# Optimization experiments

Measured on AMD Instinct MI355X. Metric: run time of the kernel, lower is better.

The kernel has to match this reference:

```python
import jax, jax.numpy as jnp
import numpy as np
from jax import lax

# pywt db4 filters. REC_LO is pywt's rec_lo; the others follow pywt's QMF relations:
# rec_hi[k] = (-1)**k * rec_lo[F-1-k]; dec_lo = rec_lo[::-1]; dec_hi = rec_hi[::-1].
REC_LO = np.array([0.23037781330885523, 0.7148465705525415, 0.6308807679295904,
                   -0.027983769416983849, -0.18703481171888114, 0.030841381835986965,
                   0.032883011666982945, -0.010597401784997278], dtype=np.float32)
F = 8
REC_HI = np.array([(-1.0) ** k * REC_LO[F - 1 - k] for k in range(F)], dtype=np.float32)
DEC_LO = REC_LO[::-1].copy()
DEC_HI = REC_HI[::-1].copy()
LEVELS = 3


def _conv(x, kern, stride=1, lhs_dilation=1, padding=((0, 0),)):
    # x: (N, 1, L) ; 1-D correlation (jax conv does NOT flip the kernel)
    k = jnp.asarray(kern, x.dtype).reshape(1, 1, -1)
    return lax.conv_general_dilated(x, k, window_strides=(stride,), padding=padding,
                                    lhs_dilation=(lhs_dilation,),
                                    dimension_numbers=('NCH', 'OIH', 'NCH'))


def dwt(x):
    # pywt single-level dwt, mode='symmetric': extend by F-1 each side, then
    # decimated convolution with dec filters. Equivalent to: drop first extended
    # sample and stride-2 correlate with reversed dec filter (= rec filter).
    xe = jnp.pad(x, ((0, 0), (0, 0), (F - 1, F - 1)), mode='symmetric')[..., 1:]
    cA = _conv(xe, REC_LO, stride=2)   # rev(DEC_LO) == REC_LO
    cD = _conv(xe, REC_HI, stride=2)   # rev(DEC_HI) == REC_HI
    return cA, cD


def idwt(a, d):
    # pywt idwt: upsample by 2 (zeros between samples, len 2L-1), full-convolve
    # with rec filters, trim F-2 from each side -> len 2L - F + 2.
    # Via dilated conv: lhs_dilation=2, pad 1 each side, correlate with rev(rec)=dec.
    ra = _conv(a, DEC_LO, lhs_dilation=2, padding=((1, 1),))
    rd = _conv(d, DEC_HI, lhs_dilation=2, padding=((1, 1),))
    return ra + rd


def waverec(coeffs):
    a = coeffs[0]
    for d in coeffs[1:]:
        if a.shape[-1] == d.shape[-1] + 1:
            a = a[..., :-1]
        a = idwt(a, d)
    return a


def setup_inputs() -> dict:
    key = jax.random.key(0)
    x = jax.random.normal(key, (32, 64, 8192), dtype=jnp.float32)
    return {"x": x}


def reference(x):
    B, C, n = x.shape
    a = x.reshape(B * C, 1, n)
    details = []
    for _ in range(LEVELS):
        a, d = dwt(a)
        details.append(d)
    coeffs = [a] + details[::-1]  # [cA_L, cD_L, ..., cD_1] as in pywt.wavedec
    bands = []
    for i in range(LEVELS + 1):
        kept = [c if j == i else jnp.zeros_like(c) for j, c in enumerate(coeffs)]
        rec = waverec(kept)[..., :n]
        bands.append(rec.reshape(B, C, n))
    return tuple(bands)
```

## Files before the change

kernel.cpp:

```cpp
#include <hip/hip_runtime.h>


#define T     1024
#define N0    8192
#define L1    4099
#define L2    2053
#define L3    1030
#define NROWS 2048

#define RL0 0.23037781330885523f
#define RL1 0.7148465705525415f
#define RL2 0.6308807679295904f
#define RL3 (-0.02798376941698385f)
#define RL4 (-0.18703481171888114f)
#define RL5 0.030841381835986965f
#define RL6 0.032883011666982945f
#define RL7 (-0.010597401784997278f)

__device__ __forceinline__ void fwd_interior(const float* __restrict__ s, int tHi,
                                             float* __restrict__ dstA,
                                             float* __restrict__ dstD, int tid)
{
    const float lo[8] = {RL0, RL1, RL2, RL3, RL4, RL5, RL6, RL7};
    const float hi[8] = {RL7, -RL6, RL5, -RL4, RL3, -RL2, RL1, -RL0};
    const float4* s4 = (const float4*)s;
    for (int t = 2 + tid; t < tHi; t += T) {
        float4 q0 = s4[t - 2], q1 = s4[t - 1], q2 = s4[t];
        float w[10] = {q0.z, q0.w, q1.x, q1.y, q1.z, q1.w,
                       q2.x, q2.y, q2.z, q2.w};
        float sa0 = 0.f, sd0 = 0.f, sa1 = 0.f, sd1 = 0.f;
#pragma unroll
        for (int k = 0; k < 8; ++k) {
            sa0 = fmaf(w[k],     lo[k], sa0);
            sd0 = fmaf(w[k],     hi[k], sd0);
            sa1 = fmaf(w[k + 2], lo[k], sa1);
            sd1 = fmaf(w[k + 2], hi[k], sd1);
        }
        ((float2*)dstA)[t] = make_float2(sa0, sa1);
        ((float2*)dstD)[t] = make_float2(sd0, sd1);
    }
}

__device__ __forceinline__ void fwd_edges(const float* __restrict__ s, int n, int Lout, int tHi,
                                          float* __restrict__ dstA,
                                          float* __restrict__ dstD, int tid)
{
    const float lo[8] = {RL0, RL1, RL2, RL3, RL4, RL5, RL6, RL7};
    const float hi[8] = {RL7, -RL6, RL5, -RL4, RL3, -RL2, RL1, -RL0};
    const int ub = 2 * tHi;
    const int tot = 4 + (Lout - ub);
    if (tid < tot) {
        int i = (tid < 4) ? tid : ub + (tid - 4);
        int j0 = 2 * i - 6;
        float sa = 0.f, sd = 0.f;
#pragma unroll
        for (int t = 0; t < 8; ++t) {
            int m = j0 + t;
            m = (m < 0) ? (-1 - m) : m;
            m = (m >= n) ? (2 * n - 1 - m) : m;
            float v = s[m];
            sa = fmaf(v, lo[t], sa);
            sd = fmaf(v, hi[t], sd);
        }
        dstA[i] = sa;
        dstD[i] = sd;
    }
}

__device__ __forceinline__ void upconv_mid(const float* __restrict__ s, float* __restrict__ dst,
                                           int L,
                                           float o0, float o1, float o2, float o3,
                                           float e0, float e1, float e2, float e3, int tid)
{
    const float2* s2 = (const float2*)s;
    const int cnt = L - 3, P2 = cnt >> 1;
    for (int t = tid; t < P2; t += T) {
        float2 u0 = s2[t], u1 = s2[t + 1];
        float s4 = s[2 * t + 4];
        float a0 = u0.x, a1 = u0.y, a2 = u1.x, a3 = u1.y;
        float ev0 = a0 * e0 + a1 * e1 + a2 * e2 + a3 * e3;
        float od0 = a0 * o0 + a1 * o1 + a2 * o2 + a3 * o3;
        float ev1 = a1 * e0 + a2 * e1 + a3 * e2 + s4 * e3;
        float od1 = a1 * o0 + a2 * o1 + a3 * o2 + s4 * o3;
        ((float4*)dst)[t] = make_float4(ev0, od0, ev1, od1);
    }
    if ((cnt & 1) && tid == 0) {
        int p = cnt - 1;
        float s0 = s[p], s1 = s[p + 1], sc = s[p + 2], s3 = s[p + 3];
        float ev = s0 * e0 + s1 * e1 + sc * e2 + s3 * e3;
        float od = s0 * o0 + s1 * o1 + sc * o2 + s3 * o3;
        *(float2*)&dst[2 * p] = make_float2(ev, od);
    }
}

__device__ __forceinline__ void upconv_final(const float* __restrict__ s, float* __restrict__ g,
                                             float o0, float o1, float o2, float o3,
                                             float e0, float e1, float e2, float e3, int tid)
{
    const float2* s2 = (const float2*)s;
    for (int q = tid; q < N0 / 4; q += T) {
        float2 u0 = s2[q], u1 = s2[q + 1];
        float s4 = s[2 * q + 4];
        float a0 = u0.x, a1 = u0.y, a2 = u1.x, a3 = u1.y;
        float4 o;
        o.x = a0 * e0 + a1 * e1 + a2 * e2 + a3 * e3;
        o.y = a0 * o0 + a1 * o1 + a2 * o2 + a3 * o3;
        o.z = a1 * e0 + a2 * e1 + a3 * e2 + s4 * e3;
        o.w = a1 * o0 + a2 * o1 + a3 * o2 + s4 * o3;
        ((float4*)g)[q] = o;
    }
}

#define POOL_F 14400

__global__ __launch_bounds__(T) void wavelet_bands(const float* __restrict__ x,
                                                   float* __restrict__ out)
{
    __shared__ float buf[POOL_F];
    const int tid = threadIdx.x;
    const int row = blockIdx.x;

    float* a1 = buf;
    float* t2 = buf;
    float* u2 = buf;
    float* d1 = buf + 4112;
    float* u1 = buf + 4112;
    float* v1 = buf + 6168;
    float* a2 = buf + 8224;
    float* v2 = buf + 8224;
    float* d2 = buf + 10280;
    float* a3 = buf + 12336;
    float* d3 = buf + 13368;

    const float* xr = x + (size_t)row * N0;
    const size_t band = (size_t)NROWS * N0;
    float* o0 = out + (size_t)row * N0;
    float* o1 = o0 + band;
    float* o2 = o0 + 2 * band;
    float* o3 = o0 + 3 * band;

    const int tHi1 = (N0 - 3) >> 2;
    const int tHi2 = (L1 - 3) >> 2;
    const int tHi3 = (L2 - 3) >> 2;

    fwd_interior(xr, tHi1, a1, d1, tid);
    fwd_edges(xr, N0, L1, tHi1, a1, d1, tid);
    __syncthreads();

    upconv_final(d1, o3, -RL0, -RL2, -RL4, -RL6, RL1, RL3, RL5, RL7, tid);
    fwd_interior(a1, tHi2, a2, d2, tid);
    fwd_edges(a1, L1, L2, tHi2, a2, d2, tid);
    __syncthreads();

    fwd_interior(a2, tHi3, a3, d3, tid);
    fwd_edges(a2, L2, L3, tHi3, a3, d3, tid);
    upconv_mid(d2, t2, L2, -RL0, -RL2, -RL4, -RL6, RL1, RL3, RL5, RL7, tid);
    __syncthreads();

    upconv_final(t2, o2, RL7, RL5, RL3, RL1, RL6, RL4, RL2, RL0, tid);
    upconv_mid(a3, u1, L3, RL7, RL5, RL3, RL1, RL6, RL4, RL2, RL0, tid);
    upconv_mid(d3, v1, L3, -RL0, -RL2, -RL4, -RL6, RL1, RL3, RL5, RL7, tid);
    __syncthreads();

    upconv_mid(u1, u2, L2, RL7, RL5, RL3, RL1, RL6, RL4, RL2, RL0, tid);
    upconv_mid(v1, v2, L2, RL7, RL5, RL3, RL1, RL6, RL4, RL2, RL0, tid);
    __syncthreads();

    upconv_final(u2, o0, RL7, RL5, RL3, RL1, RL6, RL4, RL2, RL0, tid);
    upconv_final(v2, o1, RL7, RL5, RL3, RL1, RL6, RL4, RL2, RL0, tid);
}

extern "C" void kernel_launch(void* const* d_in, const int* in_sizes, int n_in,
                              void* d_out, int out_size, void* d_ws, size_t ws_size,
                              hipStream_t stream)
{
    const float* x = (const float*)d_in[0];
    float* out = (float*)d_out;
    wavelet_bands<<<NROWS, T, 0, stream>>>(x, out);
}
```

Baseline: 317.6 us.

## Tile each row into 8 overlapping windows with halo recompute per block

Splits each 8192-sample row into eight 1024-output tiles, one tile per 256-thread block, and stages a halo-extended input window in shared memory. All three forward levels and the reconstructions are computed over local windows, recomputing the halo coefficients. The LDS footprint drops from about 57KB to about 12KB per block, so many more blocks can be resident and global loads overlap better. In exchange it does redundant halo work, makes more scalar shared-memory accesses, and adds reflect-index arithmetic to every coefficient.

```diff
diff --git a/kernel.cpp b/kernel.cpp
--- a/kernel.cpp
+++ b/kernel.cpp
@@ -1,12 +1,13 @@
 #include <hip/hip_runtime.h>
 
 
-#define T     1024
-#define N0    8192
-#define L1    4099
-#define L2    2053
-#define L3    1030
-#define NROWS 2048
+#define T      256
+#define N0     8192
+#define L1     4099
+#define L2     2053
+#define L3     1030
+#define NROWS  2048
+#define TW     1024
 
 #define RL0 0.23037781330885523f
 #define RL1 0.7148465705525415f
@@ -17,157 +18,126 @@
 #define RL6 0.032883011666982945f
 #define RL7 (-0.010597401784997278f)
 
-__device__ __forceinline__ void fwd_interior(const float* __restrict__ s, int tHi,
-                                             float* __restrict__ dstA,
-                                             float* __restrict__ dstD, int tid)
+__device__ __forceinline__ int reflect(int m, int n)
+{
+    m = (m < 0) ? (-1 - m) : m;
+    m = (m >= n) ? (2 * n - 1 - m) : m;
+    return m;
+}
+
+__device__ __forceinline__ void fwd_win(const float* __restrict__ src, int src_lo,
+                                        float* __restrict__ dstA, float* __restrict__ dstD,
+                                        int out_lo, int out_len, int Lv, int tid)
 {
     const float lo[8] = {RL0, RL1, RL2, RL3, RL4, RL5, RL6, RL7};
     const float hi[8] = {RL7, -RL6, RL5, -RL4, RL3, -RL2, RL1, -RL0};
-    const float4* s4 = (const float4*)s;
-    for (int t = 2 + tid; t < tHi; t += T) {
-        float4 q0 = s4[t - 2], q1 = s4[t - 1], q2 = s4[t];
-        float w[10] = {q0.z, q0.w, q1.x, q1.y, q1.z, q1.w,
-                       q2.x, q2.y, q2.z, q2.w};
-        float sa0 = 0.f, sd0 = 0.f, sa1 = 0.f, sd1 = 0.f;
+    for (int idx = tid; idx < out_len; idx += T) {
+        int g  = out_lo + idx;
+        int ge = reflect(g, Lv);
+        int b  = 2 * ge - 6 - src_lo;
+        float sa = 0.f, sd = 0.f;
 #pragma unroll
         for (int k = 0; k < 8; ++k) {
-            sa0 = fmaf(w[k],     lo[k], sa0);
-            sd0 = fmaf(w[k],     hi[k], sd0);
-            sa1 = fmaf(w[k + 2], lo[k], sa1);
-            sd1 = fmaf(w[k + 2], hi[k], sd1);
+            float v = src[b + k];
+            sa = fmaf(v, lo[k], sa);
+            sd = fmaf(v, hi[k], sd);
         }
-        ((float2*)dstA)[t] = make_float2(sa0, sa1);
-        ((float2*)dstD)[t] = make_float2(sd0, sd1);
+        dstA[idx] = sa;
+        dstD[idx] = sd;
     }
 }
 
-__device__ __forceinline__ void fwd_edges(const float* __restrict__ s, int n, int Lout, int tHi,
-                                          float* __restrict__ dstA,
-                                          float* __restrict__ dstD, int tid)
+__device__ __forceinline__ void up_win(const float* __restrict__ src, int src_lo,
+                                       float* __restrict__ dst, int t0, int pairs,
+                                       float o0, float o1, float o2, float o3,
+                                       float e0, float e1, float e2, float e3, int tid)
 {
-    const float lo[8] = {RL0, RL1, RL2, RL3, RL4, RL5, RL6, RL7};
-    const float hi[8] = {RL7, -RL6, RL5, -RL4, RL3, -RL2, RL1, -RL0};
-    const int ub = 2 * tHi;
-    const int tot = 4 + (Lout - ub);
-    if (tid < tot) {
-        int i = (tid < 4) ? tid : ub + (tid - 4);
-        int j0 = 2 * i - 6;
-        float sa = 0.f, sd = 0.f;
-#pragma unroll
-        for (int t = 0; t < 8; ++t) {
-            int m = j0 + t;
-            m = (m < 0) ? (-1 - m) : m;
-            m = (m >= n) ? (2 * n - 1 - m) : m;
-            float v = s[m];
-            sa = fmaf(v, lo[t], sa);
-            sd = fmaf(v, hi[t], sd);
-        }
-        dstA[i] = sa;
-        dstD[i] = sd;
+    for (int idx = tid; idx < pairs; idx += T) {
+        int b = t0 + idx - src_lo;
+        float s0 = src[b], s1 = src[b + 1], s2 = src[b + 2], s3 = src[b + 3];
+        float ev = s0 * e0 + s1 * e1 + s2 * e2 + s3 * e3;
+        float od = s0 * o0 + s1 * o1 + s2 * o2 + s3 * o3;
+        ((float2*)dst)[idx] = make_float2(ev, od);
     }
 }
 
-__device__ __forceinline__ void upconv_mid(const float* __restrict__ s, float* __restrict__ dst,
-                                           int L,
-                                           float o0, float o1, float o2, float o3,
-                                           float e0, float e1, float e2, float e3, int tid)
+__device__ __forceinline__ void fin_win(const float* __restrict__ src, int src_lo, int n0,
+                                        float* __restrict__ g,
+                                        float o0, float o1, float o2, float o3,
+                                        float e0, float e1, float e2, float e3, int tid)
 {
-    const float2* s2 = (const float2*)s;
-    const int cnt = L - 3, P2 = cnt >> 1;
-    for (int t = tid; t < P2; t += T) {
-        float2 u0 = s2[t], u1 = s2[t + 1];
-        float s4 = s[2 * t + 4];
-        float a0 = u0.x, a1 = u0.y, a2 = u1.x, a3 = u1.y;
-        float ev0 = a0 * e0 + a1 * e1 + a2 * e2 + a3 * e3;
-        float od0 = a0 * o0 + a1 * o1 + a2 * o2 + a3 * o3;
-        float ev1 = a1 * e0 + a2 * e1 + a3 * e2 + s4 * e3;
-        float od1 = a1 * o0 + a2 * o1 + a3 * o2 + s4 * o3;
-        ((float4*)dst)[t] = make_float4(ev0, od0, ev1, od1);
-    }
-    if ((cnt & 1) && tid == 0) {
-        int p = cnt - 1;
-        float s0 = s[p], s1 = s[p + 1], sc = s[p + 2], s3 = s[p + 3];
-        float ev = s0 * e0 + s1 * e1 + sc * e2 + s3 * e3;
-        float od = s0 * o0 + s1 * o1 + sc * o2 + s3 * o3;
-        *(float2*)&dst[2 * p] = make_float2(ev, od);
-    }
+    int b = (n0 >> 1) + 2 * tid - src_lo;
+    float s0 = src[b], s1 = src[b + 1], s2 = src[b + 2], s3 = src[b + 3], s4 = src[b + 4];
+    float4 o;
+    o.x = s0 * e0 + s1 * e1 + s2 * e2 + s3 * e3;
+    o.y = s0 * o0 + s1 * o1 + s2 * o2 + s3 * o3;
+    o.z = s1 * e0 + s2 * e1 + s3 * e2 + s4 * e3;
+    o.w = s1 * o0 + s2 * o1 + s3 * o2 + s4 * o3;
+    ((float4*)(g + n0))[tid] = o;
 }
 
-__device__ __forceinline__ void upconv_final(const float* __restrict__ s, float* __restrict__ g,
-                                             float o0, float o1, float o2, float o3,
-                                             float e0, float e1, float e2, float e3, int tid)
-{
-    const float2* s2 = (const float2*)s;
-    for (int q = tid; q < N0 / 4; q += T) {
-        float2 u0 = s2[q], u1 = s2[q + 1];
-        float s4 = s[2 * q + 4];
-        float a0 = u0.x, a1 = u0.y, a2 = u1.x, a3 = u1.y;
-        float4 o;
-        o.x = a0 * e0 + a1 * e1 + a2 * e2 + a3 * e3;
-        o.y = a0 * o0 + a1 * o1 + a2 * o2 + a3 * o3;
-        o.z = a1 * e0 + a2 * e1 + a3 * e2 + s4 * e3;
-        o.w = a1 * o0 + a2 * o1 + a3 * o2 + s4 * o3;
-        ((float4*)g)[q] = o;
-    }
-}
-
-#define POOL_F 14400
+#define POOL_F 3088
 
 __global__ __launch_bounds__(T) void wavelet_bands(const float* __restrict__ x,
                                                    float* __restrict__ out)
 {
     __shared__ float buf[POOL_F];
-    const int tid = threadIdx.x;
-    const int row = blockIdx.x;
+    const int tid  = threadIdx.x;
+    const int bid  = blockIdx.x;
+    const int row  = bid >> 3;
+    const int tile = bid & 7;
+    const int n0   = tile * TW;
 
-    float* a1 = buf;
-    float* t2 = buf;
-    float* u2 = buf;
-    float* d1 = buf + 4112;
-    float* u1 = buf + 4112;
-    float* v1 = buf + 6168;
-    float* a2 = buf + 8224;
-    float* v2 = buf + 8224;
-    float* d2 = buf + 10280;
-    float* a3 = buf + 12336;
-    float* d3 = buf + 13368;
+    const int lo1 = (n0 >> 1) - 18;
+    const int lo2 = (n0 >> 2) - 6;
+    const int lo3 = (n0 >> 3);
+    const int lox = n0 - 48;
+
+    float* a1w = buf;
+    float* d1w = buf + 560;
+    float* a2w = buf + 1120;
+    float* d2w = buf + 1400;
+    float* a3w = buf + 1680;
+    float* d3w = buf + 1816;
+    float* xw  = buf + 1952;
+    float* t2  = xw;
+    float* t1a = xw + 520;
+    float* t1d = xw + 784;
+    float* t2d = buf;
 
     const float* xr = x + (size_t)row * N0;
     const size_t band = (size_t)NROWS * N0;
-    float* o0 = out + (size_t)row * N0;
-    float* o1 = o0 + band;
-    float* o2 = o0 + 2 * band;
-    float* o3 = o0 + 3 * band;
+    float* o0p = out + (size_t)row * N0;
+    float* o1p = o0p + band;
+    float* o2p = o0p + 2 * band;
+    float* o3p = o0p + 3 * band;
 
-    const int tHi1 = (N0 - 3) >> 2;
-    const int tHi2 = (L1 - 3) >> 2;
-    const int tHi3 = (L2 - 3) >> 2;
-
-    fwd_interior(xr, tHi1, a1, d1, tid);
-    fwd_edges(xr, N0, L1, tHi1, a1, d1, tid);
+    for (int idx = tid; idx < 1128; idx += T)
+        xw[idx] = xr[reflect(lox + idx, N0)];
     __syncthreads();
 
-    upconv_final(d1, o3, -RL0, -RL2, -RL4, -RL6, RL1, RL3, RL5, RL7, tid);
-    fwd_interior(a1, tHi2, a2, d2, tid);
-    fwd_edges(a1, L1, L2, tHi2, a2, d2, tid);
+    fwd_win(xw, lox, a1w, d1w, lo1, 558, L1, tid);
     __syncthreads();
 
-    fwd_interior(a2, tHi3, a3, d3, tid);
-    fwd_edges(a2, L2, L3, tHi3, a3, d3, tid);
-    upconv_mid(d2, t2, L2, -RL0, -RL2, -RL4, -RL6, RL1, RL3, RL5, RL7, tid);
+    fwd_win(a1w, lo1, a2w, d2w, lo2, 276, L2, tid);
+    fin_win(d1w, lo1, n0, o3p, -RL0, -RL2, -RL4, -RL6, RL1, RL3, RL5, RL7, tid);
     __syncthreads();
 
-    upconv_final(t2, o2, RL7, RL5, RL3, RL1, RL6, RL4, RL2, RL0, tid);
-    upconv_mid(a3, u1, L3, RL7, RL5, RL3, RL1, RL6, RL4, RL2, RL0, tid);
-    upconv_mid(d3, v1, L3, -RL0, -RL2, -RL4, -RL6, RL1, RL3, RL5, RL7, tid);
+    fwd_win(a2w, lo2, a3w, d3w, lo3, 135, L3, tid);
+    up_win(d2w, lo2, t2, n0 >> 2, 258, -RL0, -RL2, -RL4, -RL6, RL1, RL3, RL5, RL7, tid);
     __syncthreads();
 
-    upconv_mid(u1, u2, L2, RL7, RL5, RL3, RL1, RL6, RL4, RL2, RL0, tid);
-    upconv_mid(v1, v2, L2, RL7, RL5, RL3, RL1, RL6, RL4, RL2, RL0, tid);
+    fin_win(t2, n0 >> 1, n0, o2p, RL7, RL5, RL3, RL1, RL6, RL4, RL2, RL0, tid);
+    up_win(a3w, lo3, t1a, n0 >> 3, 131, RL7, RL5, RL3, RL1, RL6, RL4, RL2, RL0, tid);
+    up_win(d3w, lo3, t1d, n0 >> 3, 131, -RL0, -RL2, -RL4, -RL6, RL1, RL3, RL5, RL7, tid);
     __syncthreads();
 
-    upconv_final(u2, o0, RL7, RL5, RL3, RL1, RL6, RL4, RL2, RL0, tid);
-    upconv_final(v2, o1, RL7, RL5, RL3, RL1, RL6, RL4, RL2, RL0, tid);
+    up_win(t1a, n0 >> 2, t2,  n0 >> 2, 258, RL7, RL5, RL3, RL1, RL6, RL4, RL2, RL0, tid);
+    up_win(t1d, n0 >> 2, t2d, n0 >> 2, 258, RL7, RL5, RL3, RL1, RL6, RL4, RL2, RL0, tid);
+    __syncthreads();
+
+    fin_win(t2,  n0 >> 1, n0, o0p, RL7, RL5, RL3, RL1, RL6, RL4, RL2, RL0, tid);
+    fin_win(t2d, n0 >> 1, n0, o1p, RL7, RL5, RL3, RL1, RL6, RL4, RL2, RL0, tid);
 }
 
 extern "C" void kernel_launch(void* const* d_in, const int* in_sizes, int n_in,
@@ -176,5 +146,5 @@
 {
     const float* x = (const float*)d_in[0];
     float* out = (float*)d_out;
-    wavelet_bands<<<NROWS, T, 0, stream>>>(x, out);
+    wavelet_bands<<<NROWS * 8, T, 0, stream>>>(x, out);
 }
```

New measurement: 318.8 us. About the same (+0.4%).
